# Kernel optimization log

Measured on AMD Instinct MI355X. Metric: run time of the kernel, lower is better.

## Reference

```python
import jax, jax.numpy as jnp
import numpy as np

L, B, N, C = 6, 8, 300, 20
H, W = 28, 28
GT_H, GT_W = 448, 448


def _pair_similarity(rm_b):
    # rm_b: (N, H, W). Pairwise (IoU + Dice)/2 between thresholded (>0.7) masks.
    T = (rm_b.reshape(N, H * W) > 0.7).astype(jnp.float32)
    inter = T @ T.T                                  # (N, N)
    s = T.sum(axis=1)
    union = s[:, None] + s[None, :] - inter
    tot = s[:, None] + s[None, :]
    iou = jnp.where(union == 0, 1.0, inter / jnp.where(union == 0, 1.0, union))
    dice = jnp.where(tot == 0, 1.0, 2.0 * inter / jnp.where(tot == 0, 1.0, tot))
    return 0.5 * (iou + dice)


def _cluster(S_b, cls_sc):
    # NMS-style greedy transitive expansion from the top-scoring candidate.
    # Equivalent to the torch while-loop: fin_{k+1} = {j in cand : max_{i in fin_k} S[i,j] > 0.5}
    cand = cls_sc > 0.01
    has_cand = jnp.any(cand)
    adj = S_b > 0.5                                   # (N, N) similarity graph
    seed = jnp.argmax(jnp.where(cand, cls_sc, -jnp.inf))
    fin0 = cand & adj[seed]                           # seed always included (S[seed,seed]=1)

    def cond(st):
        return st[1]

    def body(st):
        fin = st[0]
        new = cand & jnp.any(adj & fin[:, None], axis=0)
        return (new, jnp.any(new != fin))

    fin = jax.lax.while_loop(cond, body, (fin0, jnp.array(True)))[0]
    fallback = jnp.arange(N) == jnp.argmax(cls_sc)    # no candidate above 0.01 -> argmax only
    return jnp.where(has_cand, fin, fallback)


def _safe_log(x):
    # matches torch BCELoss log clamping (log clamped at -100)
    return jnp.where(x > 0, jnp.log(jnp.maximum(x, 1e-38)), -100.0)


def _forward(score_map, score, label, gt):
    # per-query CAMs, relu'd and max-normalized
    rm = jax.nn.relu(jnp.mean(score_map, axis=0).reshape(B, N, H, W))
    mx = jnp.max(rm, axis=(-2, -1), keepdims=True)
    rm = rm / (mx + 1e-6)

    S = jax.lax.stop_gradient(jax.vmap(_pair_similarity)(rm))   # (B, N, N)
    sc = jax.lax.stop_gradient(score)                            # used only in comparisons

    def pair_loss(rm_b, S_b, sc_b, gt_b, c):
        fin = _cluster(S_b, sc_b[:, c]).astype(jnp.float32)      # (N,)
        # mean over selected masks commutes with bilinear resize (linear op)
        mean_map = jnp.einsum('n,nhw->hw', fin, rm_b) / jnp.sum(fin)
        pred = jax.image.resize(mean_map, (GT_H, GT_W), method='linear')  # align_corners=False
        y = (gt_b == c + 1).astype(jnp.float32)
        return -jnp.mean(y * _safe_log(pred) + (1.0 - y) * _safe_log(1.0 - pred))

    cls = jnp.arange(C)
    per_b = jax.vmap(lambda rm_b, S_b, sc_b, gt_b:
                     jax.vmap(lambda c: pair_loss(rm_b, S_b, sc_b, gt_b, c))(cls))
    losses = per_b(rm, S, sc, gt)                                # (B, C)
    act = (label != 0).astype(jnp.float32)
    return jnp.sum(losses * act) / jnp.sum(act)


def setup_inputs() -> dict:
    key = jax.random.key(0)
    k1, k2, k3, k4 = jax.random.split(key, 4)
    return {
        'score_map': jax.random.normal(k1, (L, B, N, H * W), dtype=jnp.float32),
        'score': jax.random.uniform(k2, (B, N, C), dtype=jnp.float32),
        'label': jax.random.randint(k3, (B, C), 0, 2).astype(jnp.int32),
        'gt': jax.random.randint(k4, (B, GT_H, GT_W), 0, C + 1).astype(jnp.int32),
    }


def reference(score_map, score, label, gt):
    return _forward(score_map, score, label, gt)
```

## Files before the change

kernel.cpp:

```cpp
#include <hip/hip_runtime.h>
#include <math.h>

#define LNUM 6
#define BNUM 8
#define NNUM 300
#define CNUM 20
#define HW   784
#define HW4  196
#define GH   448
#define NW   16
#define AW   5
#define RT   16
#define NTILE 28
#define TOTBC  (BNUM*CNUM)
#define TOTBLK (TOTBC*NTILE)

__device__ float              g_rm [BNUM*NNUM*HW];
__device__ unsigned long long g_T  [BNUM*NNUM*NW];
__device__ int                g_s  [BNUM*NNUM];
__device__ unsigned long long g_adj[BNUM*NNUM*AW];
__device__ float              g_mm [BNUM*CNUM*HW];
struct PadD { double v; double pad[15]; };
struct PadI { int v;    int    pad[31]; };
__device__ PadD g_accbc[TOTBC];
__device__ PadI g_tdone[TOTBC];
__device__ int  g_bdone = 0;

__global__ void k_rm(const float* __restrict__ sm) {
    int bn  = blockIdx.x;
    int tid = threadIdx.x;
    int lane = tid & 63, wid = tid >> 6;
    __shared__ float wmax[4];
    __shared__ int   scount;
    if (tid == 0) scount = 0;
    const size_t lstr4 = (size_t)BNUM * NNUM * HW4;
    const float4* base = (const float4*)sm + (size_t)bn * HW4;
    bool act = tid < HW4;
    float4 v = {0.f, 0.f, 0.f, 0.f};
    if (act) {
        float4 a = {0.f, 0.f, 0.f, 0.f};
        #pragma unroll
        for (int l = 0; l < LNUM; ++l) {
            float4 x = base[(size_t)l * lstr4 + tid];
            a.x += x.x; a.y += x.y; a.z += x.z; a.w += x.w;
        }
        v.x = fmaxf(__fdiv_rn(a.x, 6.0f), 0.0f);
        v.y = fmaxf(__fdiv_rn(a.y, 6.0f), 0.0f);
        v.z = fmaxf(__fdiv_rn(a.z, 6.0f), 0.0f);
        v.w = fmaxf(__fdiv_rn(a.w, 6.0f), 0.0f);
    }
    float lm = fmaxf(fmaxf(v.x, v.y), fmaxf(v.z, v.w));
    #pragma unroll
    for (int off = 32; off; off >>= 1) lm = fmaxf(lm, __shfl_xor(lm, off));
    if (lane == 0) wmax[wid] = lm;
    __syncthreads();
    float mx = fmaxf(fmaxf(wmax[0], wmax[1]), fmaxf(wmax[2], wmax[3]));
    float d = mx + 1e-6f;
    float4 nv;
    nv.x = __fdiv_rn(v.x, d); nv.y = __fdiv_rn(v.y, d);
    nv.z = __fdiv_rn(v.z, d); nv.w = __fdiv_rn(v.w, d);
    if (act) ((float4*)g_rm)[(size_t)bn * HW4 + tid] = nv;
    float c[4] = {nv.x, nv.y, nv.z, nv.w};
    #pragma unroll
    for (int k = 0; k < 4; ++k) {
        bool pr = act && (c[k] > 0.7f);
        unsigned long long ball = __ballot(pr);
        if (lane == 0) {
            g_T[(size_t)bn * NW + k * 4 + wid] = ball;
            atomicAdd(&scount, __popcll(ball));
        }
    }
    __syncthreads();
    if (tid == 0) g_s[bn] = scount;
}

__global__ void k_adj() {
    int blk = blockIdx.x;
    int b = blk / NNUM;
    int tid = threadIdx.x;
    __shared__ unsigned long long Ti[NW];
    __shared__ int si_sh;
    if (tid < NW)  Ti[tid] = g_T[(size_t)blk * NW + tid];
    if (tid == NW) si_sh = g_s[blk];
    __syncthreads();
    bool a = false;
    int j = tid;
    if (j < NNUM) {
        const unsigned long long* Tj = &g_T[((size_t)b * NNUM + j) * NW];
        int inter = 0;
        #pragma unroll
        for (int w = 0; w < NW; ++w) inter += __popcll(Ti[w] & Tj[w]);
        int si = si_sh, sj = g_s[b * NNUM + j];
        int uni = si + sj - inter, tot = si + sj;
        float iou  = (uni == 0) ? 1.0f : __fdiv_rn((float)inter, (float)uni);
        float dice = (tot == 0) ? 1.0f : __fdiv_rn(2.0f * (float)inter, (float)tot);
        a = (0.5f * (iou + dice)) > 0.5f;
    }
    unsigned long long ball = __ballot(a);
    if ((tid & 63) == 0) g_adj[(size_t)blk * AW + (tid >> 6)] = ball;
}

__global__ void __launch_bounds__(320)
k_cm(const float* __restrict__ score, const int* __restrict__ label) {
    int blk = blockIdx.x;
    if (label[blk] == 0) return;
    int b = blk / CNUM, c = blk - b * CNUM;
    int tid = threadIdx.x;
    int lane = tid & 63, wid = tid >> 6;
    __shared__ unsigned long long adj_sh[NNUM][AW];
    __shared__ unsigned long long cand[AW], fin[AW], nwv[AW];
    __shared__ float wbv[AW], wbva[AW];
    __shared__ int   wbi[AW], wbia[AW];
    __shared__ int sh_has, sh_go;
    __shared__ float sh_cf;
    for (int idx = tid; idx < NNUM * AW; idx += 320)
        ((unsigned long long*)adj_sh)[idx] = g_adj[(size_t)b * NNUM * AW + idx];
    int j = tid;
    bool cb = false;
    float sc = -INFINITY;
    if (j < NNUM) {
        sc = score[((size_t)b * NNUM + j) * CNUM + c];
        cb = sc > 0.01f;
    }
    unsigned long long ball = __ballot(cb);
    if (lane == 0) cand[wid] = ball;
    float bv  = cb ? sc : -INFINITY;          int bi  = cb ? j : NNUM;
    float bva = (j < NNUM) ? sc : -INFINITY;  int bia = (j < NNUM) ? j : NNUM;
    #pragma unroll
    for (int off = 1; off < 64; off <<= 1) {
        float ov = __shfl_xor(bv, off);  int oi = __shfl_xor(bi, off);
        if (ov > bv || (ov == bv && oi < bi)) { bv = ov; bi = oi; }
        float ova = __shfl_xor(bva, off); int oia = __shfl_xor(bia, off);
        if (ova > bva || (ova == bva && oia < bia)) { bva = ova; bia = oia; }
    }
    if (lane == 0) { wbv[wid] = bv; wbi[wid] = bi; wbva[wid] = bva; wbia[wid] = bia; }
    __syncthreads();
    if (tid == 0) {
        float cv = -INFINITY; int ci = NNUM;
        float cva = -INFINITY; int cia = NNUM;
        #pragma unroll
        for (int w = 0; w < AW; ++w) {
            if (wbv[w] > cv)  { cv = wbv[w];  ci = wbi[w]; }
            if (wbva[w] > cva) { cva = wbva[w]; cia = wbia[w]; }
        }
        bool has = (cand[0] | cand[1] | cand[2] | cand[3] | cand[4]) != 0ULL;
        sh_has = has ? 1 : 0;
        if (has) {
            #pragma unroll
            for (int w = 0; w < AW; ++w) fin[w] = cand[w] & adj_sh[ci][w];
        } else {
            #pragma unroll
            for (int w = 0; w < AW; ++w)
                fin[w] = ((cia >> 6) == w) ? (1ULL << (cia & 63)) : 0ULL;
        }
    }
    __syncthreads();
    if (sh_has) {
        bool cj = cb;
        for (int it = 0; it < NNUM + 2; ++it) {
            bool nb = false;
            if (j < NNUM && cj) {
                unsigned long long o =
                    (adj_sh[j][0] & fin[0]) | (adj_sh[j][1] & fin[1]) |
                    (adj_sh[j][2] & fin[2]) | (adj_sh[j][3] & fin[3]) |
                    (adj_sh[j][4] & fin[4]);
                nb = (o != 0ULL);
            }
            unsigned long long nball = __ballot(nb);
            if (lane == 0) nwv[wid] = nball;
            __syncthreads();
            if (wid == 0) {
                bool ch = (lane < AW) && (nwv[lane] != fin[lane]);
                unsigned long long chb = __ballot(ch);
                if (lane == 0) sh_go = (chb != 0ULL) ? 1 : 0;
                if (lane < AW) fin[lane] = nwv[lane];
            }
            __syncthreads();
            if (!sh_go) break;
        }
    }
    if (tid == 0) {
        int cs = 0;
        for (int w = 0; w < AW; ++w) cs += __popcll(fin[w]);
        sh_cf = (float)cs;
    }
    __syncthreads();
    if (tid < HW4) {
        float4 a = {0.f, 0.f, 0.f, 0.f};
        for (int w = 0; w < AW; ++w) {
            unsigned long long word = fin[w];
            while (word) {
                int jj = w * 64 + (__ffsll(word) - 1);
                word &= word - 1;
                float4 r = ((const float4*)g_rm)[((size_t)b * NNUM + jj) * HW4 + tid];
                a.x += r.x; a.y += r.y; a.z += r.z; a.w += r.w;
            }
        }
        float cdiv = sh_cf;
        float4 o;
        o.x = __fdiv_rn(a.x, cdiv); o.y = __fdiv_rn(a.y, cdiv);
        o.z = __fdiv_rn(a.z, cdiv); o.w = __fdiv_rn(a.w, cdiv);
        ((float4*)g_mm)[(size_t)blk * HW4 + tid] = o;
    }
}

__global__ void __launch_bounds__(448)
k_bce(const int* __restrict__ gt, const int* __restrict__ label, float* __restrict__ out) {
    int blk = blockIdx.x;
    int bc = blk / NTILE, tile = blk - bc * NTILE;
    int tid = threadIdx.x;
    int lane = tid & 63, wid = tid >> 6;
    __shared__ float m[HW];
    __shared__ float rowY[RT * 28];
    __shared__ double wsum[7];
    __shared__ int sh_last, sh_sa;
    bool active = (label[bc] != 0);
    if (active) {
        int b = bc / CNUM, c = bc - b * CNUM;
        if (tid < HW4) ((float4*)m)[tid] = ((const float4*)g_mm)[(size_t)bc * HW4 + tid];
        __syncthreads();
        int row0 = tile * RT;
        {
            int r = tid / 28, x = tid - (tid / 28) * 28;
            int oy = row0 + r;
            float iy = fmaf((float)oy, 0.0625f, -0.46875f);
            float y0f = floorf(iy);
            float wy = iy - y0f;
            int y0 = (int)y0f;
            if (y0 < 0) { y0 = 0; wy = 0.0f; } else if (y0 > 26) { y0 = 26; wy = 1.0f; }
            float lo = m[y0 * 28 + x], hi = m[y0 * 28 + 28 + x];
            rowY[tid] = lo + wy * (hi - lo);
        }
        __syncthreads();
        double acc = 0.0;
        {
            int r = tid / 28, j = tid - (tid / 28) * 28;
            const int* gr = gt + ((size_t)b * GH + row0 + r) * GH;
            int cp1 = c + 1;
            if (j < 27) {
                float rY0 = rowY[r * 28 + j], rY1 = rowY[r * 28 + j + 1];
                float sl = rY1 - rY0;
                const int4* gp = (const int4*)(gr + 16 * j + 8);
                #pragma unroll
                for (int q = 0; q < 4; ++q) {
                    int4 g4 = gp[q];
                    #pragma unroll
                    for (int uu = 0; uu < 4; ++uu) {
                        int k = q * 4 + uu;
                        int gv = (uu == 0) ? g4.x : (uu == 1) ? g4.y : (uu == 2) ? g4.z : g4.w;
                        float wk = fmaf((float)k, 0.0625f, 0.03125f);
                        float pred = rY0 + wk * sl;
                        float xv = (gv == cp1) ? pred : 1.0f - pred;
                        float lg = __logf(fmaxf(xv, 1.175494351e-38f));
                        acc += (double)((xv > 0.0f) ? lg : -100.0f);
                    }
                }
            } else {
                #pragma unroll
                for (int side = 0; side < 2; ++side) {
                    float pred = rowY[r * 28 + (side ? 27 : 0)];
                    const int4* gp = (const int4*)(gr + (side ? 440 : 0));
                    int4 a0 = gp[0], a1 = gp[1];
                    int np = (a0.x == cp1) + (a0.y == cp1) + (a0.z == cp1) + (a0.w == cp1)
                           + (a1.x == cp1) + (a1.y == cp1) + (a1.z == cp1) + (a1.w == cp1);
                    float om = 1.0f - pred;
                    float lgp = (pred > 0.0f) ? __logf(fmaxf(pred, 1.175494351e-38f)) : -100.0f;
                    float lgn = (om   > 0.0f) ? __logf(fmaxf(om,   1.175494351e-38f)) : -100.0f;
                    acc += (double)lgp * (double)np + (double)lgn * (double)(8 - np);
                }
            }
        }
        #pragma unroll
        for (int off = 32; off; off >>= 1) acc += __shfl_xor(acc, off);
        if (lane == 0) wsum[wid] = acc;
        __syncthreads();
    }
    if (tid == 0) {
        sh_last = 0;
        if (active) {
            double s = 0.0;
            #pragma unroll
            for (int w = 0; w < 7; ++w) s += wsum[w];
            atomicAdd(&g_accbc[bc].v, -s * (1.0 / (448.0 * 448.0)));
            asm volatile("s_waitcnt vmcnt(0)" ::: "memory");
        }
        int t = __hip_atomic_fetch_add(&g_tdone[bc].v, 1, __ATOMIC_RELAXED, __HIP_MEMORY_SCOPE_AGENT);
        if (t == NTILE - 1) {
            atomicExch(&g_tdone[bc].v, 0);
            asm volatile("s_waitcnt vmcnt(0)" ::: "memory");
            int d = __hip_atomic_fetch_add(&g_bdone, 1, __ATOMIC_RELAXED, __HIP_MEMORY_SCOPE_AGENT);
            if (d == TOTBC - 1) {
                atomicExch(&g_bdone, 0);
                sh_last = 1;
            }
        }
    }
    __syncthreads();
    if (sh_last) {
        if (tid == 0) sh_sa = 0;
        __syncthreads();
        double s = 0.0;
        if (tid < TOTBC) {
            unsigned long long bits = atomicExch((unsigned long long*)&g_accbc[tid].v, 0ULL);
            s = __longlong_as_double(bits);
            if (label[tid] != 0) atomicAdd(&sh_sa, 1);
        }
        #pragma unroll
        for (int off = 32; off; off >>= 1) s += __shfl_xor(s, off);
        if (lane == 0) wsum[wid] = s;
        __syncthreads();
        if (tid == 0) {
            double tot = 0.0;
            #pragma unroll
            for (int w = 0; w < 7; ++w) tot += wsum[w];
            out[0] = (float)(tot / (double)sh_sa);
        }
    }
}

extern "C" void kernel_launch(void* const* d_in, const int* in_sizes, int n_in,
                              void* d_out, int out_size, void* d_ws, size_t ws_size,
                              hipStream_t stream) {
    const float* smap  = (const float*)d_in[0];
    const float* score = (const float*)d_in[1];
    const int*   label = (const int*)d_in[2];
    const int*   gt    = (const int*)d_in[3];
    float* out = (float*)d_out;

    hipLaunchKernelGGL(k_rm,  dim3(BNUM * NNUM), dim3(256), 0, stream, smap);
    hipLaunchKernelGGL(k_adj, dim3(BNUM * NNUM), dim3(320), 0, stream);
    hipLaunchKernelGGL(k_cm,  dim3(TOTBC),       dim3(320), 0, stream, score, label);
    hipLaunchKernelGGL(k_bce, dim3(TOTBLK),      dim3(448), 0, stream, gt, label, out);
}
```

Before: 54.23 us.

## Fuse clustering and BCE kernels into one block per (batch,class)

```diff
diff --git a/kernel.cpp b/kernel.cpp
--- a/kernel.cpp
+++ b/kernel.cpp
@@ -13,17 +13,15 @@
 #define RT   16
 #define NTILE 28
 #define TOTBC  (BNUM*CNUM)
-#define TOTBLK (TOTBC*NTILE)
-
-__device__ float              g_rm [BNUM*NNUM*HW];
-__device__ unsigned long long g_T  [BNUM*NNUM*NW];
-__device__ int                g_s  [BNUM*NNUM];
-__device__ unsigned long long g_adj[BNUM*NNUM*AW];
-__device__ float              g_mm [BNUM*CNUM*HW];
+
+typedef unsigned long long ull;
+
+__device__ float g_rm [BNUM*NNUM*HW];
+__device__ ull   g_T  [BNUM*NNUM*NW];
+__device__ int   g_s  [BNUM*NNUM];
+__device__ ull   g_adj[BNUM*NNUM*AW];
 struct PadD { double v; double pad[15]; };
-struct PadI { int v;    int    pad[31]; };
 __device__ PadD g_accbc[TOTBC];
-__device__ PadI g_tdone[TOTBC];
 __device__ int  g_bdone = 0;
 
 __global__ void k_rm(const float* __restrict__ sm) {
@@ -64,7 +62,7 @@
     #pragma unroll
     for (int k = 0; k < 4; ++k) {
         bool pr = act && (c[k] > 0.7f);
-        unsigned long long ball = __ballot(pr);
+        ull ball = __ballot(pr);
         if (lane == 0) {
             g_T[(size_t)bn * NW + k * 4 + wid] = ball;
             atomicAdd(&scount, __popcll(ball));
@@ -78,7 +76,7 @@
     int blk = blockIdx.x;
     int b = blk / NNUM;
     int tid = threadIdx.x;
-    __shared__ unsigned long long Ti[NW];
+    __shared__ ull Ti[NW];
     __shared__ int si_sh;
     if (tid < NW)  Ti[tid] = g_T[(size_t)blk * NW + tid];
     if (tid == NW) si_sh = g_s[blk];
@@ -86,7 +84,7 @@
     bool a = false;
     int j = tid;
     if (j < NNUM) {
-        const unsigned long long* Tj = &g_T[((size_t)b * NNUM + j) * NW];
+        const ull* Tj = &g_T[((size_t)b * NNUM + j) * NW];
         int inter = 0;
         #pragma unroll
         for (int w = 0; w < NW; ++w) inter += __popcll(Ti[w] & Tj[w]);
@@ -96,151 +94,148 @@
         float dice = (tot == 0) ? 1.0f : __fdiv_rn(2.0f * (float)inter, (float)tot);
         a = (0.5f * (iou + dice)) > 0.5f;
     }
-    unsigned long long ball = __ballot(a);
+    ull ball = __ballot(a);
     if ((tid & 63) == 0) g_adj[(size_t)blk * AW + (tid >> 6)] = ball;
 }
 
-__global__ void __launch_bounds__(320)
-k_cm(const float* __restrict__ score, const int* __restrict__ label) {
-    int blk = blockIdx.x;
-    if (label[blk] == 0) return;
-    int b = blk / CNUM, c = blk - b * CNUM;
+__global__ void __launch_bounds__(896, 1)
+k_cmbce(const float* __restrict__ score, const int* __restrict__ label,
+        const int* __restrict__ gt, float* __restrict__ out) {
+    int bc = blockIdx.x;
+    int b = bc / CNUM, c = bc - b * CNUM;
     int tid = threadIdx.x;
     int lane = tid & 63, wid = tid >> 6;
-    __shared__ unsigned long long adj_sh[NNUM][AW];
-    __shared__ unsigned long long cand[AW], fin[AW], nwv[AW];
+    bool active = (label[bc] != 0);
+
+    __shared__ ull adj_sh[NNUM][AW];
+    __shared__ ull cand[AW], fin[AW], nwv[AW];
     __shared__ float wbv[AW], wbva[AW];
     __shared__ int   wbi[AW], wbia[AW];
-    __shared__ int sh_has, sh_go;
+    __shared__ int sh_has, sh_go, sh_last, sh_sa;
     __shared__ float sh_cf;
-    for (int idx = tid; idx < NNUM * AW; idx += 320)
-        ((unsigned long long*)adj_sh)[idx] = g_adj[(size_t)b * NNUM * AW + idx];
-    int j = tid;
-    bool cb = false;
-    float sc = -INFINITY;
-    if (j < NNUM) {
-        sc = score[((size_t)b * NNUM + j) * CNUM + c];
-        cb = sc > 0.01f;
-    }
-    unsigned long long ball = __ballot(cb);
-    if (lane == 0) cand[wid] = ball;
-    float bv  = cb ? sc : -INFINITY;          int bi  = cb ? j : NNUM;
-    float bva = (j < NNUM) ? sc : -INFINITY;  int bia = (j < NNUM) ? j : NNUM;
-    #pragma unroll
-    for (int off = 1; off < 64; off <<= 1) {
-        float ov = __shfl_xor(bv, off);  int oi = __shfl_xor(bi, off);
-        if (ov > bv || (ov == bv && oi < bi)) { bv = ov; bi = oi; }
-        float ova = __shfl_xor(bva, off); int oia = __shfl_xor(bia, off);
-        if (ova > bva || (ova == bva && oia < bia)) { bva = ova; bia = oia; }
-    }
-    if (lane == 0) { wbv[wid] = bv; wbi[wid] = bi; wbva[wid] = bva; wbia[wid] = bia; }
-    __syncthreads();
-    if (tid == 0) {
-        float cv = -INFINITY; int ci = NNUM;
-        float cva = -INFINITY; int cia = NNUM;
-        #pragma unroll
-        for (int w = 0; w < AW; ++w) {
-            if (wbv[w] > cv)  { cv = wbv[w];  ci = wbi[w]; }
-            if (wbva[w] > cva) { cva = wbva[w]; cia = wbia[w]; }
-        }
-        bool has = (cand[0] | cand[1] | cand[2] | cand[3] | cand[4]) != 0ULL;
-        sh_has = has ? 1 : 0;
-        if (has) {
+    __shared__ float m[HW];
+    __shared__ float rowY[2 * RT * 28];
+    __shared__ double wsum[14];
+
+    if (active) {
+        for (int idx = tid; idx < NNUM * AW; idx += 896)
+            ((ull*)adj_sh)[idx] = g_adj[(size_t)b * NNUM * AW + idx];
+        int j = tid;
+        bool cb = false;
+        if (wid < AW) {
+            float sc = -INFINITY;
+            if (j < NNUM) {
+                sc = score[((size_t)b * NNUM + j) * CNUM + c];
+                cb = sc > 0.01f;
+            }
+            ull ball = __ballot(cb);
+            if (lane == 0) cand[wid] = ball;
+            float bv  = cb ? sc : -INFINITY;          int bi  = cb ? j : NNUM;
+            float bva = (j < NNUM) ? sc : -INFINITY;  int bia = (j < NNUM) ? j : NNUM;
             #pragma unroll
-            for (int w = 0; w < AW; ++w) fin[w] = cand[w] & adj_sh[ci][w];
-        } else {
+            for (int off = 1; off < 64; off <<= 1) {
+                float ov = __shfl_xor(bv, off);  int oi = __shfl_xor(bi, off);
+                if (ov > bv || (ov == bv && oi < bi)) { bv = ov; bi = oi; }
+                float ova = __shfl_xor(bva, off); int oia = __shfl_xor(bia, off);
+                if (ova > bva || (ova == bva && oia < bia)) { bva = ova; bia = oia; }
+            }
+            if (lane == 0) { wbv[wid] = bv; wbi[wid] = bi; wbva[wid] = bva; wbia[wid] = bia; }
+        }
+        __syncthreads();
+        if (tid == 0) {
+            float cv = -INFINITY; int ci = NNUM;
+            float cva = -INFINITY; int cia = NNUM;
             #pragma unroll
-            for (int w = 0; w < AW; ++w)
-                fin[w] = ((cia >> 6) == w) ? (1ULL << (cia & 63)) : 0ULL;
-        }
-    }
-    __syncthreads();
-    if (sh_has) {
-        bool cj = cb;
-        for (int it = 0; it < NNUM + 2; ++it) {
-            bool nb = false;
-            if (j < NNUM && cj) {
-                unsigned long long o =
-                    (adj_sh[j][0] & fin[0]) | (adj_sh[j][1] & fin[1]) |
-                    (adj_sh[j][2] & fin[2]) | (adj_sh[j][3] & fin[3]) |
-                    (adj_sh[j][4] & fin[4]);
-                nb = (o != 0ULL);
-            }
-            unsigned long long nball = __ballot(nb);
-            if (lane == 0) nwv[wid] = nball;
+            for (int w = 0; w < AW; ++w) {
+                if (wbv[w] > cv)   { cv = wbv[w];   ci = wbi[w]; }
+                if (wbva[w] > cva) { cva = wbva[w]; cia = wbia[w]; }
+            }
+            bool has = (cand[0] | cand[1] | cand[2] | cand[3] | cand[4]) != 0ULL;
+            sh_has = has ? 1 : 0;
+            if (has) {
+                #pragma unroll
+                for (int w = 0; w < AW; ++w) fin[w] = cand[w] & adj_sh[ci][w];
+            } else {
+                #pragma unroll
+                for (int w = 0; w < AW; ++w)
+                    fin[w] = ((cia >> 6) == w) ? (1ULL << (cia & 63)) : 0ULL;
+            }
+        }
+        __syncthreads();
+        if (sh_has) {
+            for (int it = 0; it < NNUM + 2; ++it) {
+                if (wid < AW) {
+                    bool nb = false;
+                    if (j < NNUM && cb) {
+                        ull o = (adj_sh[j][0] & fin[0]) | (adj_sh[j][1] & fin[1]) |
+                                (adj_sh[j][2] & fin[2]) | (adj_sh[j][3] & fin[3]) |
+                                (adj_sh[j][4] & fin[4]);
+                        nb = (o != 0ULL);
+                    }
+                    ull nball = __ballot(nb);
+                    if (lane == 0) nwv[wid] = nball;
+                }
+                __syncthreads();
+                if (wid == 0) {
+                    bool ch = (lane < AW) && (nwv[lane] != fin[lane]);
+                    ull chb = __ballot(ch);
+                    if (lane == 0) sh_go = (chb != 0ULL) ? 1 : 0;
+                    if (lane < AW) fin[lane] = nwv[lane];
+                }
+                __syncthreads();
+                if (!sh_go) break;
+            }
+        }
+        if (tid == 0) {
+            int cs = 0;
+            for (int w = 0; w < AW; ++w) cs += __popcll(fin[w]);
+            sh_cf = (float)cs;
+        }
+        __syncthreads();
+        if (tid < HW4) {
+            float4 a = {0.f, 0.f, 0.f, 0.f};
+            for (int w = 0; w < AW; ++w) {
+                ull word = fin[w];
+                while (word) {
+                    int jj = w * 64 + (__ffsll(word) - 1);
+                    word &= word - 1;
+                    float4 r = ((const float4*)g_rm)[((size_t)b * NNUM + jj) * HW4 + tid];
+                    a.x += r.x; a.y += r.y; a.z += r.z; a.w += r.w;
+                }
+            }
+            float cdiv = sh_cf;
+            float4 o;
+            o.x = __fdiv_rn(a.x, cdiv); o.y = __fdiv_rn(a.y, cdiv);
+            o.z = __fdiv_rn(a.z, cdiv); o.w = __fdiv_rn(a.w, cdiv);
+            ((float4*)m)[tid] = o;
+        }
+        __syncthreads();
+        int half = (tid >= 448) ? 1 : 0;
+        int t448 = tid - half * 448;
+        int r  = t448 / 28, jx = t448 - r * 28;
+        float* rY = rowY + half * (RT * 28);
+        int cp1 = c + 1;
+        double accd = 0.0;
+        for (int tt = 0; tt < 14; ++tt) {
+            int tile = tt * 2 + half;
+            int row0 = tile * RT;
             __syncthreads();
-            if (wid == 0) {
-                bool ch = (lane < AW) && (nwv[lane] != fin[lane]);
-                unsigned long long chb = __ballot(ch);
-                if (lane == 0) sh_go = (chb != 0ULL) ? 1 : 0;
-                if (lane < AW) fin[lane] = nwv[lane];
+            {
+                int oy = row0 + r;
+                float iy = fmaf((float)oy, 0.0625f, -0.46875f);
+                float y0f = floorf(iy);
+                float wy = iy - y0f;
+                int y0 = (int)y0f;
+                if (y0 < 0) { y0 = 0; wy = 0.0f; } else if (y0 > 26) { y0 = 26; wy = 1.0f; }
+                float lo = m[y0 * 28 + jx], hi = m[y0 * 28 + 28 + jx];
+                rY[t448] = lo + wy * (hi - lo);
             }
             __syncthreads();
-            if (!sh_go) break;
-        }
-    }
-    if (tid == 0) {
-        int cs = 0;
-        for (int w = 0; w < AW; ++w) cs += __popcll(fin[w]);
-        sh_cf = (float)cs;
-    }
-    __syncthreads();
-    if (tid < HW4) {
-        float4 a = {0.f, 0.f, 0.f, 0.f};
-        for (int w = 0; w < AW; ++w) {
-            unsigned long long word = fin[w];
-            while (word) {
-                int jj = w * 64 + (__ffsll(word) - 1);
-                word &= word - 1;
-                float4 r = ((const float4*)g_rm)[((size_t)b * NNUM + jj) * HW4 + tid];
-                a.x += r.x; a.y += r.y; a.z += r.z; a.w += r.w;
-            }
-        }
-        float cdiv = sh_cf;
-        float4 o;
-        o.x = __fdiv_rn(a.x, cdiv); o.y = __fdiv_rn(a.y, cdiv);
-        o.z = __fdiv_rn(a.z, cdiv); o.w = __fdiv_rn(a.w, cdiv);
-        ((float4*)g_mm)[(size_t)blk * HW4 + tid] = o;
-    }
-}
-
-__global__ void __launch_bounds__(448)
-k_bce(const int* __restrict__ gt, const int* __restrict__ label, float* __restrict__ out) {
-    int blk = blockIdx.x;
-    int bc = blk / NTILE, tile = blk - bc * NTILE;
-    int tid = threadIdx.x;
-    int lane = tid & 63, wid = tid >> 6;
-    __shared__ float m[HW];
-    __shared__ float rowY[RT * 28];
-    __shared__ double wsum[7];
-    __shared__ int sh_last, sh_sa;
-    bool active = (label[bc] != 0);
-    if (active) {
-        int b = bc / CNUM, c = bc - b * CNUM;
-        if (tid < HW4) ((float4*)m)[tid] = ((const float4*)g_mm)[(size_t)bc * HW4 + tid];
-        __syncthreads();
-        int row0 = tile * RT;
-        {
-            int r = tid / 28, x = tid - (tid / 28) * 28;
-            int oy = row0 + r;
-            float iy = fmaf((float)oy, 0.0625f, -0.46875f);
-            float y0f = floorf(iy);
-            float wy = iy - y0f;
-            int y0 = (int)y0f;
-            if (y0 < 0) { y0 = 0; wy = 0.0f; } else if (y0 > 26) { y0 = 26; wy = 1.0f; }
-            float lo = m[y0 * 28 + x], hi = m[y0 * 28 + 28 + x];
-            rowY[tid] = lo + wy * (hi - lo);
-        }
-        __syncthreads();
-        double acc = 0.0;
-        {
-            int r = tid / 28, j = tid - (tid / 28) * 28;
             const int* gr = gt + ((size_t)b * GH + row0 + r) * GH;
-            int cp1 = c + 1;
-            if (j < 27) {
-                float rY0 = rowY[r * 28 + j], rY1 = rowY[r * 28 + j + 1];
+            if (jx < 27) {
+                float rY0 = rY[r * 28 + jx], rY1 = rY[r * 28 + jx + 1];
                 float sl = rY1 - rY0;
-                const int4* gp = (const int4*)(gr + 16 * j + 8);
+                const int4* gp = (const int4*)(gr + 16 * jx + 8);
                 #pragma unroll
                 for (int q = 0; q < 4; ++q) {
                     int4 g4 = gp[q];
@@ -252,13 +247,13 @@
                         float pred = rY0 + wk * sl;
                         float xv = (gv == cp1) ? pred : 1.0f - pred;
                         float lg = __logf(fmaxf(xv, 1.175494351e-38f));
-                        acc += (double)((xv > 0.0f) ? lg : -100.0f);
+                        accd += (double)((xv > 0.0f) ? lg : -100.0f);
                     }
                 }
             } else {
                 #pragma unroll
                 for (int side = 0; side < 2; ++side) {
-                    float pred = rowY[r * 28 + (side ? 27 : 0)];
+                    float pred = rY[r * 28 + (side ? 27 : 0)];
                     const int4* gp = (const int4*)(gr + (side ? 440 : 0));
                     int4 a0 = gp[0], a1 = gp[1];
                     int np = (a0.x == cp1) + (a0.y == cp1) + (a0.z == cp1) + (a0.w == cp1)
@@ -266,33 +261,28 @@
                     float om = 1.0f - pred;
                     float lgp = (pred > 0.0f) ? __logf(fmaxf(pred, 1.175494351e-38f)) : -100.0f;
                     float lgn = (om   > 0.0f) ? __logf(fmaxf(om,   1.175494351e-38f)) : -100.0f;
-                    acc += (double)lgp * (double)np + (double)lgn * (double)(8 - np);
+                    accd += (double)lgp * (double)np + (double)lgn * (double)(8 - np);
                 }
             }
         }
         #pragma unroll
-        for (int off = 32; off; off >>= 1) acc += __shfl_xor(acc, off);
-        if (lane == 0) wsum[wid] = acc;
-        __syncthreads();
+        for (int off = 32; off; off >>= 1) accd += __shfl_xor(accd, off);
+        if (lane == 0) wsum[wid] = accd;
+        __syncthreads();
+        if (tid == 0) {
+            double s = 0.0;
+            #pragma unroll
+            for (int w = 0; w < 14; ++w) s += wsum[w];
+            atomicAdd(&g_accbc[bc].v, -s * (1.0 / (448.0 * 448.0)));
+            asm volatile("s_waitcnt vmcnt(0)" ::: "memory");
+        }
     }
     if (tid == 0) {
         sh_last = 0;
-        if (active) {
-            double s = 0.0;
-            #pragma unroll
-            for (int w = 0; w < 7; ++w) s += wsum[w];
-            atomicAdd(&g_accbc[bc].v, -s * (1.0 / (448.0 * 448.0)));
-            asm volatile("s_waitcnt vmcnt(0)" ::: "memory");
-        }
-        int t = __hip_atomic_fetch_add(&g_tdone[bc].v, 1, __ATOMIC_RELAXED, __HIP_MEMORY_SCOPE_AGENT);
-        if (t == NTILE - 1) {
-            atomicExch(&g_tdone[bc].v, 0);
-            asm volatile("s_waitcnt vmcnt(0)" ::: "memory");
-            int d = __hip_atomic_fetch_add(&g_bdone, 1, __ATOMIC_RELAXED, __HIP_MEMORY_SCOPE_AGENT);
-            if (d == TOTBC - 1) {
-                atomicExch(&g_bdone, 0);
-                sh_last = 1;
-            }
+        int d = __hip_atomic_fetch_add(&g_bdone, 1, __ATOMIC_RELAXED, __HIP_MEMORY_SCOPE_AGENT);
+        if (d == TOTBC - 1) {
+            atomicExch(&g_bdone, 0);
+            sh_last = 1;
         }
     }
     __syncthreads();
@@ -301,7 +291,7 @@
         __syncthreads();
         double s = 0.0;
         if (tid < TOTBC) {
-            unsigned long long bits = atomicExch((unsigned long long*)&g_accbc[tid].v, 0ULL);
+            ull bits = atomicExch((ull*)&g_accbc[tid].v, 0ULL);
             s = __longlong_as_double(bits);
             if (label[tid] != 0) atomicAdd(&sh_sa, 1);
         }
@@ -312,7 +302,7 @@
         if (tid == 0) {
             double tot = 0.0;
             #pragma unroll
-            for (int w = 0; w < 7; ++w) tot += wsum[w];
+            for (int w = 0; w < 14; ++w) tot += wsum[w];
             out[0] = (float)(tot / (double)sh_sa);
         }
     }
@@ -327,8 +317,7 @@
     const int*   gt    = (const int*)d_in[3];
     float* out = (float*)d_out;
 
-    hipLaunchKernelGGL(k_rm,  dim3(BNUM * NNUM), dim3(256), 0, stream, smap);
-    hipLaunchKernelGGL(k_adj, dim3(BNUM * NNUM), dim3(320), 0, stream);
-    hipLaunchKernelGGL(k_cm,  dim3(TOTBC),       dim3(320), 0, stream, score, label);
-    hipLaunchKernelGGL(k_bce, dim3(TOTBLK),      dim3(448), 0, stream, gt, label, out);
+    hipLaunchKernelGGL(k_rm,    dim3(BNUM * NNUM), dim3(256), 0, stream, smap);
+    hipLaunchKernelGGL(k_adj,   dim3(BNUM * NNUM), dim3(320), 0, stream);
+    hipLaunchKernelGGL(k_cmbce, dim3(TOTBC),       dim3(896), 0, stream, score, label, gt, out);
 }
```

After: 83.15 us. 1.53x slower.

## Pack gt labels to bytes in k_rm and process two row tiles per BCE block

Applied to the files above, without the earlier changes.

```diff
diff --git a/kernel.cpp b/kernel.cpp
--- a/kernel.cpp
+++ b/kernel.cpp
@@ -11,24 +11,43 @@
 #define NW   16
 #define AW   5
 #define RT   16
-#define NTILE 28
+#define NT2  14
 #define TOTBC  (BNUM*CNUM)
-#define TOTBLK (TOTBC*NTILE)
-
-__device__ float              g_rm [BNUM*NNUM*HW];
-__device__ unsigned long long g_T  [BNUM*NNUM*NW];
-__device__ int                g_s  [BNUM*NNUM];
-__device__ unsigned long long g_adj[BNUM*NNUM*AW];
-__device__ float              g_mm [BNUM*CNUM*HW];
+#define RM_UNITS (BNUM*NNUM)
+#define CVT_BLKS 392
+#define BCEBLK  (TOTBC*NT2)
+
+typedef unsigned long long ull;
+
+__device__ float         g_rm [BNUM*NNUM*HW];
+__device__ ull           g_T  [BNUM*NNUM*NW];
+__device__ int           g_s  [BNUM*NNUM];
+__device__ ull           g_adj[BNUM*NNUM*AW];
+__device__ float         g_mm [TOTBC*HW];
+__device__ unsigned char g_gt8[BNUM*GH*GH];
 struct PadD { double v; double pad[15]; };
 struct PadI { int v;    int    pad[31]; };
 __device__ PadD g_accbc[TOTBC];
 __device__ PadI g_tdone[TOTBC];
 __device__ int  g_bdone = 0;
 
-__global__ void k_rm(const float* __restrict__ sm) {
+__global__ void k_rm(const float* __restrict__ sm, const int* __restrict__ gt) {
     int bn  = blockIdx.x;
     int tid = threadIdx.x;
+    if (bn >= RM_UNITS) {
+        int g = bn - RM_UNITS;
+        const int4* gp = (const int4*)gt + (size_t)g * 1024;
+        unsigned* op = (unsigned*)g_gt8 + (size_t)g * 1024;
+        #pragma unroll
+        for (int q = 0; q < 4; ++q) {
+            int idx = q * 256 + tid;
+            int4 v = gp[idx];
+            unsigned w = (unsigned)(v.x & 255) | ((unsigned)(v.y & 255) << 8) |
+                         ((unsigned)(v.z & 255) << 16) | ((unsigned)(v.w & 255) << 24);
+            op[idx] = w;
+        }
+        return;
+    }
     int lane = tid & 63, wid = tid >> 6;
     __shared__ float wmax[4];
     __shared__ int   scount;
@@ -64,7 +83,7 @@
     #pragma unroll
     for (int k = 0; k < 4; ++k) {
         bool pr = act && (c[k] > 0.7f);
-        unsigned long long ball = __ballot(pr);
+        ull ball = __ballot(pr);
         if (lane == 0) {
             g_T[(size_t)bn * NW + k * 4 + wid] = ball;
             atomicAdd(&scount, __popcll(ball));
@@ -78,7 +97,7 @@
     int blk = blockIdx.x;
     int b = blk / NNUM;
     int tid = threadIdx.x;
-    __shared__ unsigned long long Ti[NW];
+    __shared__ ull Ti[NW];
     __shared__ int si_sh;
     if (tid < NW)  Ti[tid] = g_T[(size_t)blk * NW + tid];
     if (tid == NW) si_sh = g_s[blk];
@@ -86,7 +105,7 @@
     bool a = false;
     int j = tid;
     if (j < NNUM) {
-        const unsigned long long* Tj = &g_T[((size_t)b * NNUM + j) * NW];
+        const ull* Tj = &g_T[((size_t)b * NNUM + j) * NW];
         int inter = 0;
         #pragma unroll
         for (int w = 0; w < NW; ++w) inter += __popcll(Ti[w] & Tj[w]);
@@ -96,7 +115,7 @@
         float dice = (tot == 0) ? 1.0f : __fdiv_rn(2.0f * (float)inter, (float)tot);
         a = (0.5f * (iou + dice)) > 0.5f;
     }
-    unsigned long long ball = __ballot(a);
+    ull ball = __ballot(a);
     if ((tid & 63) == 0) g_adj[(size_t)blk * AW + (tid >> 6)] = ball;
 }
 
@@ -107,14 +126,14 @@
     int b = blk / CNUM, c = blk - b * CNUM;
     int tid = threadIdx.x;
     int lane = tid & 63, wid = tid >> 6;
-    __shared__ unsigned long long adj_sh[NNUM][AW];
-    __shared__ unsigned long long cand[AW], fin[AW], nwv[AW];
+    __shared__ ull adj_sh[NNUM][AW];
+    __shared__ ull cand[AW], fin[AW], nwv[AW];
     __shared__ float wbv[AW], wbva[AW];
     __shared__ int   wbi[AW], wbia[AW];
     __shared__ int sh_has, sh_go;
     __shared__ float sh_cf;
     for (int idx = tid; idx < NNUM * AW; idx += 320)
-        ((unsigned long long*)adj_sh)[idx] = g_adj[(size_t)b * NNUM * AW + idx];
+        ((ull*)adj_sh)[idx] = g_adj[(size_t)b * NNUM * AW + idx];
     int j = tid;
     bool cb = false;
     float sc = -INFINITY;
@@ -122,7 +141,7 @@
         sc = score[((size_t)b * NNUM + j) * CNUM + c];
         cb = sc > 0.01f;
     }
-    unsigned long long ball = __ballot(cb);
+    ull ball = __ballot(cb);
     if (lane == 0) cand[wid] = ball;
     float bv  = cb ? sc : -INFINITY;          int bi  = cb ? j : NNUM;
     float bva = (j < NNUM) ? sc : -INFINITY;  int bia = (j < NNUM) ? j : NNUM;
@@ -140,7 +159,7 @@
         float cva = -INFINITY; int cia = NNUM;
         #pragma unroll
         for (int w = 0; w < AW; ++w) {
-            if (wbv[w] > cv)  { cv = wbv[w];  ci = wbi[w]; }
+            if (wbv[w] > cv)   { cv = wbv[w];   ci = wbi[w]; }
             if (wbva[w] > cva) { cva = wbva[w]; cia = wbia[w]; }
         }
         bool has = (cand[0] | cand[1] | cand[2] | cand[3] | cand[4]) != 0ULL;
@@ -156,22 +175,20 @@
     }
     __syncthreads();
     if (sh_has) {
-        bool cj = cb;
         for (int it = 0; it < NNUM + 2; ++it) {
             bool nb = false;
-            if (j < NNUM && cj) {
-                unsigned long long o =
-                    (adj_sh[j][0] & fin[0]) | (adj_sh[j][1] & fin[1]) |
-                    (adj_sh[j][2] & fin[2]) | (adj_sh[j][3] & fin[3]) |
-                    (adj_sh[j][4] & fin[4]);
+            if (j < NNUM && cb) {
+                ull o = (adj_sh[j][0] & fin[0]) | (adj_sh[j][1] & fin[1]) |
+                        (adj_sh[j][2] & fin[2]) | (adj_sh[j][3] & fin[3]) |
+                        (adj_sh[j][4] & fin[4]);
                 nb = (o != 0ULL);
             }
-            unsigned long long nball = __ballot(nb);
+            ull nball = __ballot(nb);
             if (lane == 0) nwv[wid] = nball;
             __syncthreads();
             if (wid == 0) {
                 bool ch = (lane < AW) && (nwv[lane] != fin[lane]);
-                unsigned long long chb = __ballot(ch);
+                ull chb = __ballot(ch);
                 if (lane == 0) sh_go = (chb != 0ULL) ? 1 : 0;
                 if (lane < AW) fin[lane] = nwv[lane];
             }
@@ -188,7 +205,7 @@
     if (tid < HW4) {
         float4 a = {0.f, 0.f, 0.f, 0.f};
         for (int w = 0; w < AW; ++w) {
-            unsigned long long word = fin[w];
+            ull word = fin[w];
             while (word) {
                 int jj = w * 64 + (__ffsll(word) - 1);
                 word &= word - 1;
@@ -205,9 +222,9 @@
 }
 
 __global__ void __launch_bounds__(448)
-k_bce(const int* __restrict__ gt, const int* __restrict__ label, float* __restrict__ out) {
+k_bce(const int* __restrict__ label, float* __restrict__ out) {
     int blk = blockIdx.x;
-    int bc = blk / NTILE, tile = blk - bc * NTILE;
+    int bc = blk / NT2, tt = blk - bc * NT2;
     int tid = threadIdx.x;
     int lane = tid & 63, wid = tid >> 6;
     __shared__ float m[HW];
@@ -217,52 +234,50 @@
     bool active = (label[bc] != 0);
     if (active) {
         int b = bc / CNUM, c = bc - b * CNUM;
+        int cp1 = c + 1;
+        int r = tid / 28, jx = tid - (tid / 28) * 28;
         if (tid < HW4) ((float4*)m)[tid] = ((const float4*)g_mm)[(size_t)bc * HW4 + tid];
-        __syncthreads();
-        int row0 = tile * RT;
-        {
-            int r = tid / 28, x = tid - (tid / 28) * 28;
-            int oy = row0 + r;
-            float iy = fmaf((float)oy, 0.0625f, -0.46875f);
-            float y0f = floorf(iy);
-            float wy = iy - y0f;
-            int y0 = (int)y0f;
-            if (y0 < 0) { y0 = 0; wy = 0.0f; } else if (y0 > 26) { y0 = 26; wy = 1.0f; }
-            float lo = m[y0 * 28 + x], hi = m[y0 * 28 + 28 + x];
-            rowY[tid] = lo + wy * (hi - lo);
-        }
-        __syncthreads();
         double acc = 0.0;
-        {
-            int r = tid / 28, j = tid - (tid / 28) * 28;
-            const int* gr = gt + ((size_t)b * GH + row0 + r) * GH;
-            int cp1 = c + 1;
-            if (j < 27) {
-                float rY0 = rowY[r * 28 + j], rY1 = rowY[r * 28 + j + 1];
+        #pragma unroll
+        for (int t2 = 0; t2 < 2; ++t2) {
+            int tile = tt * 2 + t2;
+            int row0 = tile * RT;
+            __syncthreads();
+            {
+                int oy = row0 + r;
+                float iy = fmaf((float)oy, 0.0625f, -0.46875f);
+                float y0f = floorf(iy);
+                float wy = iy - y0f;
+                int y0 = (int)y0f;
+                if (y0 < 0) { y0 = 0; wy = 0.0f; } else if (y0 > 26) { y0 = 26; wy = 1.0f; }
+                float lo = m[y0 * 28 + jx], hi = m[y0 * 28 + 28 + jx];
+                rowY[tid] = lo + wy * (hi - lo);
+            }
+            __syncthreads();
+            const unsigned char* g8 = g_gt8 + ((size_t)b * GH + row0 + r) * GH;
+            if (jx < 27) {
+                float rY0 = rowY[tid], rY1 = rowY[tid + 1];
                 float sl = rY1 - rY0;
-                const int4* gp = (const int4*)(gr + 16 * j + 8);
+                ull w0 = *(const ull*)(g8 + 16 * jx + 8);
+                ull w1 = *(const ull*)(g8 + 16 * jx + 16);
                 #pragma unroll
-                for (int q = 0; q < 4; ++q) {
-                    int4 g4 = gp[q];
-                    #pragma unroll
-                    for (int uu = 0; uu < 4; ++uu) {
-                        int k = q * 4 + uu;
-                        int gv = (uu == 0) ? g4.x : (uu == 1) ? g4.y : (uu == 2) ? g4.z : g4.w;
-                        float wk = fmaf((float)k, 0.0625f, 0.03125f);
-                        float pred = rY0 + wk * sl;
-                        float xv = (gv == cp1) ? pred : 1.0f - pred;
-                        float lg = __logf(fmaxf(xv, 1.175494351e-38f));
-                        acc += (double)((xv > 0.0f) ? lg : -100.0f);
-                    }
+                for (int k = 0; k < 16; ++k) {
+                    int gv = (int)((k < 8 ? (w0 >> (8 * k)) : (w1 >> (8 * (k - 8)))) & 255);
+                    float wk = fmaf((float)k, 0.0625f, 0.03125f);
+                    float pred = rY0 + wk * sl;
+                    float xv = (gv == cp1) ? pred : 1.0f - pred;
+                    float lg = __logf(fmaxf(xv, 1.175494351e-38f));
+                    acc += (double)((xv > 0.0f) ? lg : -100.0f);
                 }
             } else {
                 #pragma unroll
                 for (int side = 0; side < 2; ++side) {
                     float pred = rowY[r * 28 + (side ? 27 : 0)];
-                    const int4* gp = (const int4*)(gr + (side ? 440 : 0));
-                    int4 a0 = gp[0], a1 = gp[1];
-                    int np = (a0.x == cp1) + (a0.y == cp1) + (a0.z == cp1) + (a0.w == cp1)
-                           + (a1.x == cp1) + (a1.y == cp1) + (a1.z == cp1) + (a1.w == cp1);
+                    ull w = *(const ull*)(g8 + (side ? 440 : 0));
+                    int np = 0;
+                    #pragma unroll
+                    for (int uu = 0; uu < 8; ++uu)
+                        np += (((w >> (8 * uu)) & 255) == (unsigned)cp1);
                     float om = 1.0f - pred;
                     float lgp = (pred > 0.0f) ? __logf(fmaxf(pred, 1.175494351e-38f)) : -100.0f;
                     float lgn = (om   > 0.0f) ? __logf(fmaxf(om,   1.175494351e-38f)) : -100.0f;
@@ -274,18 +289,18 @@
         for (int off = 32; off; off >>= 1) acc += __shfl_xor(acc, off);
         if (lane == 0) wsum[wid] = acc;
         __syncthreads();
-    }
-    if (tid == 0) {
-        sh_last = 0;
-        if (active) {
+        if (tid == 0) {
             double s = 0.0;
             #pragma unroll
             for (int w = 0; w < 7; ++w) s += wsum[w];
             atomicAdd(&g_accbc[bc].v, -s * (1.0 / (448.0 * 448.0)));
             asm volatile("s_waitcnt vmcnt(0)" ::: "memory");
         }
+    }
+    if (tid == 0) {
+        sh_last = 0;
         int t = __hip_atomic_fetch_add(&g_tdone[bc].v, 1, __ATOMIC_RELAXED, __HIP_MEMORY_SCOPE_AGENT);
-        if (t == NTILE - 1) {
+        if (t == NT2 - 1) {
             atomicExch(&g_tdone[bc].v, 0);
             asm volatile("s_waitcnt vmcnt(0)" ::: "memory");
             int d = __hip_atomic_fetch_add(&g_bdone, 1, __ATOMIC_RELAXED, __HIP_MEMORY_SCOPE_AGENT);
@@ -301,7 +316,7 @@
         __syncthreads();
         double s = 0.0;
         if (tid < TOTBC) {
-            unsigned long long bits = atomicExch((unsigned long long*)&g_accbc[tid].v, 0ULL);
+            ull bits = atomicExch((ull*)&g_accbc[tid].v, 0ULL);
             s = __longlong_as_double(bits);
             if (label[tid] != 0) atomicAdd(&sh_sa, 1);
         }
@@ -327,8 +342,8 @@
     const int*   gt    = (const int*)d_in[3];
     float* out = (float*)d_out;
 
-    hipLaunchKernelGGL(k_rm,  dim3(BNUM * NNUM), dim3(256), 0, stream, smap);
-    hipLaunchKernelGGL(k_adj, dim3(BNUM * NNUM), dim3(320), 0, stream);
-    hipLaunchKernelGGL(k_cm,  dim3(TOTBC),       dim3(320), 0, stream, score, label);
-    hipLaunchKernelGGL(k_bce, dim3(TOTBLK),      dim3(448), 0, stream, gt, label, out);
-}
+    hipLaunchKernelGGL(k_rm,  dim3(RM_UNITS + CVT_BLKS), dim3(256), 0, stream, smap, gt);
+    hipLaunchKernelGGL(k_adj, dim3(BNUM * NNUM),         dim3(320), 0, stream);
+    hipLaunchKernelGGL(k_cm,  dim3(TOTBC),               dim3(320), 0, stream, score, label);
+    hipLaunchKernelGGL(k_bce, dim3(BCEBLK),              dim3(448), 0, stream, label, out);
+}
```

New measurement: 57.10 us. 1.05x slower.
